# Performance work log

Measured on AMD Instinct MI355X. Metric: run time of the kernel, lower is better.

The kernel has to match this reference:

```python
import jax, jax.numpy as jnp
import numpy as np

B, N, D_IN, H, F = 2, 2048, 512, 8, 64
NEG_SLOPE = 0.2


def setup_inputs() -> dict:
    key = jax.random.key(0)
    k0, k1, k2, k3 = jax.random.split(key, 4)
    nodes = jax.random.normal(k0, (B, N, D_IN), dtype=jnp.float32)
    edges = jax.random.randint(k1, (B, N, N, 1), 0, 2).astype(jnp.int32)
    # ensure every node has at least one neighbor (self-loop) so softmax is finite
    idx = jnp.arange(N)
    edges = edges.at[:, idx, idx, :].set(1)
    W = jax.random.normal(k2, (D_IN, H * F), dtype=jnp.float32) * 0.02
    a = jax.random.normal(k3, (2 * F,), dtype=jnp.float32) * 0.02
    return {"nodes": nodes, "edges": edges, "W": W, "a": a}


def reference(nodes, edges, W, a):
    b, n, _ = nodes.shape
    mapped = (nodes @ W).reshape(b, n, H, F)  # [B,N,H,F]
    # additive attention: attn([m_i ; m_j]) = a_l . m_i + a_r . m_j
    a_l, a_r = a[:F], a[F:]
    el = jnp.einsum('bnhf,f->bnh', mapped, a_l)
    er = jnp.einsum('bnhf,f->bnh', mapped, a_r)
    scores = jax.nn.leaky_relu(el[:, :, None, :] + er[:, None, :, :], negative_slope=NEG_SLOPE)  # [B,N,N,H]
    mask = edges != 0  # [B,N,N,1] broadcasts over heads
    scores = jnp.where(mask, scores, -jnp.inf)
    attn_weights = jax.nn.softmax(scores, axis=2)  # softmax over neighbors j
    attn_res = jnp.einsum('bijh,bjhf->bihf', attn_weights, mapped)  # [B,N,H,F]
    # is_concat=False path: mean over heads, then sigmoid
    return jax.nn.sigmoid(attn_res.mean(axis=2))  # [B,N,F]
```

## Files before the change

### kernel.cpp

```cpp
#include <hip/hip_runtime.h>
#include <hip/hip_bf16.h>
#include <math.h>

#define Bq   2
#define Nq   2048
#define DIN  512
#define Hq   8
#define Fq   64
#define NEG  0.2f

using short8 = __attribute__((ext_vector_type(8))) short;
using half8  = __attribute__((ext_vector_type(8))) _Float16;
using half2v = __attribute__((ext_vector_type(2))) _Float16;
using f32x4  = __attribute__((ext_vector_type(4))) float;

__device__ inline unsigned int bf16_rne(float x) {
    unsigned int u = __float_as_uint(x);
    u += 0x7fffu + ((u >> 16) & 1u);
    return u >> 16;
}
__device__ inline unsigned int f16u(float x) {
    union { _Float16 h; unsigned short u; } cv;
    cv.h = (_Float16)x;
    return (unsigned int)cv.u;
}

#define AFRAG_BLOCKS 256
#define WFRAG_BLOCKS 128

__global__ __launch_bounds__(256) void prep_kernel(
    const float* __restrict__ nodes, ushort* __restrict__ Afrag,
    const float* __restrict__ W,     ushort* __restrict__ Wfrag)
{
    __shared__ __align__(16) char smem[16 * 516 * 4];
    const int bid = blockIdx.x;
    const int t   = threadIdx.x;

    if (bid < AFRAG_BLOCKS) {
        float (*As)[516] = (float(*)[516])smem;
        const int mt = bid;
        {
            const int row = t >> 4, c = t & 15;
#pragma unroll
            for (int i = 0; i < 8; i++) {
                float4 v = *(const float4*)&nodes[((size_t)mt * 16 + row) * DIN + (c + i * 16) * 4];
                *(float4*)&As[row][(c + i * 16) * 4] = v;
            }
        }
        __syncthreads();
        const int lane = t & 63, ksg = t >> 6;
        const int quad = lane >> 4, l15 = lane & 15;
#pragma unroll
        for (int k2 = 0; k2 < 4; k2++) {
            int ks = ksg * 4 + k2;
            const float* src = &As[l15][ks * 32 + quad * 8];
            float4 f0 = *(const float4*)src;
            float4 f1 = *(const float4*)(src + 4);
            uint4 pk;
            pk.x = bf16_rne(f0.x) | (bf16_rne(f0.y) << 16);
            pk.y = bf16_rne(f0.z) | (bf16_rne(f0.w) << 16);
            pk.z = bf16_rne(f1.x) | (bf16_rne(f1.y) << 16);
            pk.w = bf16_rne(f1.z) | (bf16_rne(f1.w) << 16);
            *(uint4*)(Afrag + ((size_t)(mt * 16 + ks) * 64 + lane) * 8) = pk;
        }
        return;
    }

    {
        float (*Ws)[68] = (float(*)[68])smem;
        const int id = bid - AFRAG_BLOCKS;
        const int ks = id & 15, h = id >> 4;
        {
            const int row = t >> 3, c = t & 7;
            const float* src = &W[(size_t)(ks * 32 + row) * (Hq * Fq) + h * 64 + c * 8];
            float4 v0 = *(const float4*)src;
            float4 v1 = *(const float4*)(src + 4);
            *(float4*)&Ws[row][c * 8]     = v0;
            *(float4*)&Ws[row][c * 8 + 4] = v1;
        }
        __syncthreads();
        const int lane = t & 63, nf = t >> 6;
        const int quad = lane >> 4, l15 = lane & 15;
        float f[8];
#pragma unroll
        for (int jj = 0; jj < 8; jj++) f[jj] = Ws[quad * 8 + jj][nf * 16 + l15];
        uint4 pk;
        pk.x = bf16_rne(f[0]) | (bf16_rne(f[1]) << 16);
        pk.y = bf16_rne(f[2]) | (bf16_rne(f[3]) << 16);
        pk.z = bf16_rne(f[4]) | (bf16_rne(f[5]) << 16);
        pk.w = bf16_rne(f[6]) | (bf16_rne(f[7]) << 16);
        *(uint4*)(Wfrag + (((size_t)(h * 16 + ks) * 4 + nf) * 64 + lane) * 8) = pk;
    }
}

#define GEMM_BLOCKS 512
#define PACK_BLOCKS 1024

__global__ __launch_bounds__(256) void work_kernel(
    const ushort* __restrict__ Afrag, const ushort* __restrict__ Wfrag,
    const float*  __restrict__ avec,
    ushort* __restrict__ Vfrag,
    float* __restrict__ el_t,
    float* __restrict__ er_t,
    ushort* __restrict__ Epk,
    ushort* __restrict__ Fpk,
    const int* __restrict__ edges, uint2* __restrict__ ebTB)
{
    const int bid = blockIdx.x;
    const int t   = threadIdx.x;

    if (bid >= GEMM_BLOCKS) {
        int gid = (bid - GEMM_BLOCKS) * 256 + t;
        int i  = gid & 2047;
        int jw = (gid >> 11) & 63;
        int b  = gid >> 17;
        const int4* ep = (const int4*)(edges + (((size_t)b * Nq + i) * Nq + jw * 32));
        int4 v[8];
#pragma unroll
        for (int c = 0; c < 8; c++) v[c] = ep[c];
#pragma unroll
        for (int q = 0; q < 4; q++) {
            unsigned int lo = 0, hi = 0;
            lo |= v[2*q].x   ? 0x000000FFu : 0u;  lo |= v[2*q].y   ? 0x0000FF00u : 0u;
            lo |= v[2*q].z   ? 0x00FF0000u : 0u;  lo |= v[2*q].w   ? 0xFF000000u : 0u;
            hi |= v[2*q+1].x ? 0x000000FFu : 0u;  hi |= v[2*q+1].y ? 0x0000FF00u : 0u;
            hi |= v[2*q+1].z ? 0x00FF0000u : 0u;  hi |= v[2*q+1].w ? 0xFF000000u : 0u;
            uint2 w; w.x = lo; w.y = hi;
            ebTB[((size_t)(b * 256 + jw * 4 + q)) * 2048 + i] = w;
        }
        return;
    }

    const int lane = t & 63;
    const int wv   = t >> 6;
    const int quad = lane >> 4;
    const int l15  = lane & 15;
    const int h    = bid >> 6;
    const int mt   = (bid & 63) * 4 + wv;
    const int row0 = mt * 16;

    const ushort* ap = Afrag + (size_t)mt * 8192 + lane * 8;
    const ushort* bp = Wfrag + (size_t)h * 32768 + lane * 8;

    f32x4 zero4 = {0.f, 0.f, 0.f, 0.f};
    f32x4 acc[4] = {zero4, zero4, zero4, zero4};

    short8 a0, a1, b0[4], b1[4];
    a0 = *(const short8*)(ap);
#pragma unroll
    for (int nf = 0; nf < 4; nf++) b0[nf] = *(const short8*)(bp + nf * 512);

    for (int ks = 0; ks < 16; ks += 2) {
        a1 = *(const short8*)(ap + (ks + 1) * 512);
#pragma unroll
        for (int nf = 0; nf < 4; nf++) b1[nf] = *(const short8*)(bp + (ks + 1) * 2048 + nf * 512);
#pragma unroll
        for (int nf = 0; nf < 4; nf++)
            acc[nf] = __builtin_amdgcn_mfma_f32_16x16x32_bf16(a0, b0[nf], acc[nf], 0, 0, 0);
        a0 = *(const short8*)(ap + (ks + 2) * 512);
#pragma unroll
        for (int nf = 0; nf < 4; nf++) b0[nf] = *(const short8*)(bp + (ks + 2) * 2048 + nf * 512);
#pragma unroll
        for (int nf = 0; nf < 4; nf++)
            acc[nf] = __builtin_amdgcn_mfma_f32_16x16x32_bf16(a1, b1[nf], acc[nf], 0, 0, 0);
    }

    float aL[4], aR[4];
#pragma unroll
    for (int nf = 0; nf < 4; nf++) {
        aL[nf] = avec[nf * 16 + l15];
        aR[nf] = avec[Fq + nf * 16 + l15];
    }
    const int bb = row0 >> 11;
    const int bh = bb * Hq + h;
#pragma unroll
    for (int r = 0; r < 4; r++) {
        float pl = acc[0][r] * aL[0] + acc[1][r] * aL[1] + acc[2][r] * aL[2] + acc[3][r] * aL[3];
        float pr = acc[0][r] * aR[0] + acc[1][r] * aR[1] + acc[2][r] * aR[2] + acc[3][r] * aR[3];
#pragma unroll
        for (int off = 1; off < 16; off <<= 1) {
            pl += __shfl_xor(pl, off, 64);
            pr += __shfl_xor(pr, off, 64);
        }
        if (l15 == 0) {
            int n = (row0 + quad * 4 + r) & (Nq - 1);
            el_t[(size_t)bh * Nq + n] = pl;
            er_t[(size_t)bh * Nq + n] = pr;
            Epk[(size_t)bh * Nq + n] = (ushort)f16u(__expf(pr));
            Fpk[(size_t)bh * Nq + n] = (ushort)f16u(__expf(NEG * pr));
        }
    }

    const int n_base = row0 & (Nq - 1);
    const int sblk   = n_base >> 5;
    const int quadp  = ((wv & 1) << 1) | (quad >> 1);
    const int jj0    = (quad & 1) * 4;
#pragma unroll
    for (int nf = 0; nf < 4; nf++) {
        uint2 pk;
        pk.x = f16u(acc[nf][0]) | (f16u(acc[nf][1]) << 16);
        pk.y = f16u(acc[nf][2]) | (f16u(acc[nf][3]) << 16);
        size_t off = ((((size_t)bh * 64 + sblk) * 4 + nf) * 64 + quadp * 16 + l15) * 8 + jj0;
        *(uint2*)(Vfrag + off) = pk;
    }
}

__global__ __launch_bounds__(256, 2) void attn_kernel(
    const float* __restrict__ el_t, const float* __restrict__ er_t,
    const ushort* __restrict__ Epk, const ushort* __restrict__ Fpk,
    const ushort* __restrict__ Vfrag,
    const uint2* __restrict__ ebTB, ushort* __restrict__ attn)
{
    const int lane = threadIdx.x & 63;
    const int kh   = threadIdx.x >> 6;
    const int quad = lane >> 4;
    const int l15  = lane & 15;
    const int bid  = blockIdx.x;
    const int it   = bid & 31;
    const int h    = (bid >> 5) & 7;
    const int b    = bid >> 8;
    const int bh   = b * Hq + h;
    const int i0   = it * 64;

    __shared__ float smax[4];
    __shared__ float lds_l[4][4][16];
    __shared__ __align__(16) float lds_acc[4][4][4][64][4];

    const float* errow = er_t + (size_t)bh * Nq;
    float mx = -INFINITY;
#pragma unroll
    for (int ii = 0; ii < 8; ii++) mx = fmaxf(mx, errow[threadIdx.x + ii * 256]);
#pragma unroll
    for (int off = 32; off > 0; off >>= 1) mx = fmaxf(mx, __shfl_xor(mx, off, 64));
    if (lane == 0) smax[kh] = mx;
    __syncthreads();
    const float emax = fmaxf(fmaxf(smax[0], smax[1]), fmaxf(smax[2], smax[3]));

    union HU { unsigned int u; half2v h; };
    HU AA2[4], CC2[4];
#pragma unroll
    for (int rs = 0; rs < 4; rs++) {
        float elv = el_t[(size_t)bh * Nq + i0 + rs * 16 + l15];
        float xm  = elv + emax;
        float m   = fmaxf(xm, NEG * xm);
        unsigned int a16 = f16u(__expf(elv - m));
        unsigned int c16 = f16u(__expf(NEG * elv - m));
        AA2[rs].u = a16 | (a16 << 16);
        CC2[rs].u = c16 | (c16 << 16);
    }

    const ushort* Ep = Epk + (size_t)bh * Nq + kh * 512;
    const ushort* Fp = Fpk + (size_t)bh * Nq + kh * 512;
    const ushort* vp = Vfrag + (size_t)bh * 131072 + kh * 32768 + lane * 8;
    const uint2*  mp = ebTB + ((size_t)(b * 256 + kh * 64 + quad)) * 2048 + i0 + l15;

    f32x4 zero4 = {0.f, 0.f, 0.f, 0.f};
    f32x4 acc[4][4];
    f32x4 accl[4];
#pragma unroll
    for (int rs = 0; rs < 4; rs++) {
        accl[rs] = zero4;
#pragma unroll
        for (int nf = 0; nf < 4; nf++) acc[rs][nf] = zero4;
    }

    const _Float16 one16 = (_Float16)1.0f;
    const half8 onesv = {one16, one16, one16, one16, one16, one16, one16, one16};

    for (int s = 0; s < 16; s++) {
        half8 vb0 = *(const half8*)(vp + s * 2048);
        half8 vb1 = *(const half8*)(vp + s * 2048 + 512);
        half8 vb2 = *(const half8*)(vp + s * 2048 + 1024);
        half8 vb3 = *(const half8*)(vp + s * 2048 + 1536);
        uint2 mbs[4];
#pragma unroll
        for (int rs = 0; rs < 4; rs++) mbs[rs] = mp[(size_t)s * 8192 + rs * 16];
        uint4 ev = *(const uint4*)(Ep + s * 32 + quad * 8);
        uint4 fv = *(const uint4*)(Fp + s * 32 + quad * 8);
        unsigned int ee[4] = {ev.x, ev.y, ev.z, ev.w};
        unsigned int ff[4] = {fv.x, fv.y, fv.z, fv.w};

#pragma unroll
        for (int rs = 0; rs < 4; rs++) {
            union AFU { half8 h8; unsigned int w4[4]; } af;
#pragma unroll
            for (int pp = 0; pp < 4; pp++) {
                HU e, f, pe, pf, P;
                e.u = ee[pp];
                f.u = ff[pp];
                pe.h = AA2[rs].h * e.h;
                pf.h = CC2[rs].h * f.h;
                P.h = __builtin_elementwise_max(pe.h, pf.h);
                unsigned int msrc = (pp < 2) ? mbs[rs].x : mbs[rs].y;
                unsigned int msel = (pp & 1) ? 0x03030202u : 0x01010000u;
                af.w4[pp] = P.u & __builtin_amdgcn_perm(0u, msrc, msel);
            }
            acc[rs][0] = __builtin_amdgcn_mfma_f32_16x16x32_f16(af.h8, vb0, acc[rs][0], 0, 0, 0);
            acc[rs][1] = __builtin_amdgcn_mfma_f32_16x16x32_f16(af.h8, vb1, acc[rs][1], 0, 0, 0);
            acc[rs][2] = __builtin_amdgcn_mfma_f32_16x16x32_f16(af.h8, vb2, acc[rs][2], 0, 0, 0);
            acc[rs][3] = __builtin_amdgcn_mfma_f32_16x16x32_f16(af.h8, vb3, acc[rs][3], 0, 0, 0);
            accl[rs]   = __builtin_amdgcn_mfma_f32_16x16x32_f16(af.h8, onesv, accl[rs], 0, 0, 0);
        }
    }

#pragma unroll
    for (int rs = 0; rs < 4; rs++)
#pragma unroll
        for (int nf = 0; nf < 4; nf++)
            *(f32x4*)&lds_acc[kh][rs][nf][lane][0] = acc[rs][nf];
    if (l15 == 0) {
#pragma unroll
        for (int rs = 0; rs < 4; rs++)
#pragma unroll
            for (int r = 0; r < 4; r++)
                lds_l[kh][rs][quad * 4 + r] = accl[rs][r];
    }
    __syncthreads();

    const int rs = kh;
    f32x4 facc[4] = {zero4, zero4, zero4, zero4};
#pragma unroll
    for (int k2 = 0; k2 < 4; k2++)
#pragma unroll
        for (int nf = 0; nf < 4; nf++) {
            f32x4 v = *(const f32x4*)&lds_acc[k2][rs][nf][lane][0];
            facc[nf][0] += v[0]; facc[nf][1] += v[1];
            facc[nf][2] += v[2]; facc[nf][3] += v[3];
        }
    float rl[4];
#pragma unroll
    for (int r = 0; r < 4; r++) {
        float sl = 0.f;
#pragma unroll
        for (int k2 = 0; k2 < 4; k2++) sl += lds_l[k2][rs][quad * 4 + r];
        rl[r] = 1.0f / sl;
    }
#pragma unroll
    for (int nf = 0; nf < 4; nf++)
#pragma unroll
        for (int r = 0; r < 4; r++)
            attn[(((size_t)b * Nq + i0 + rs * 16 + quad * 4 + r) * Hq + h) * Fq + nf * 16 + l15]
                = (ushort)f16u(facc[nf][r] * rl[r]);
}

__global__ __launch_bounds__(256) void out_kernel(
    const ushort* __restrict__ attn, float* __restrict__ out)
{
    const int idx = blockIdx.x * 256 + threadIdx.x;
    const int f   = idx & 63;
    const int bn  = idx >> 6;
    const ushort* p = attn + (size_t)bn * Hq * Fq + f;
    float s = 0.f;
#pragma unroll
    for (int h = 0; h < Hq; h++) {
        union { ushort u; _Float16 h16; } cv;
        cv.u = p[h * Fq];
        s += (float)cv.h16;
    }
    s *= (1.f / Hq);
    out[idx] = 1.f / (1.f + __expf(-s));
}

extern "C" void kernel_launch(void* const* d_in, const int* in_sizes, int n_in,
                              void* d_out, int out_size, void* d_ws, size_t ws_size,
                              hipStream_t stream) {
    const float* nodes = (const float*)d_in[0];
    const int*   edges = (const int*)d_in[1];
    const float* W     = (const float*)d_in[2];
    const float* a     = (const float*)d_in[3];
    float* out = (float*)d_out;

    char* ws = (char*)d_ws;
    ushort* Afrag = (ushort*)ws;           ws += (size_t)Bq * Nq * DIN * 2;
    ushort* Wfrag = (ushort*)ws;           ws += (size_t)DIN * Hq * Fq * 2;
    ushort* Vfrag = (ushort*)ws;           ws += (size_t)Bq * Hq * Nq * Fq * 2;
    float*  el_t  = (float*)ws;            ws += (size_t)Bq * Hq * Nq * 4;
    float*  er_t  = (float*)ws;            ws += (size_t)Bq * Hq * Nq * 4;
    ushort* Epk   = (ushort*)ws;           ws += (size_t)Bq * Hq * Nq * 2;
    ushort* Fpk   = (ushort*)ws;           ws += (size_t)Bq * Hq * Nq * 2;
    uint2*  ebTB  = (uint2*)ws;            ws += (size_t)Bq * Nq * Nq;
    ushort* attn  = (ushort*)ws;

    prep_kernel<<<AFRAG_BLOCKS + WFRAG_BLOCKS, 256, 0, stream>>>(nodes, Afrag, W, Wfrag);
    work_kernel<<<GEMM_BLOCKS + PACK_BLOCKS, 256, 0, stream>>>(
        Afrag, Wfrag, a, Vfrag, el_t, er_t, Epk, Fpk, edges, ebTB);
    attn_kernel<<<Bq * Hq * (Nq / 64), 256, 0, stream>>>(el_t, er_t, Epk, Fpk, Vfrag, ebTB, attn);
    out_kernel<<<(Bq * Nq * Fq) / 256, 256, 0, stream>>>(attn, out);
}
```

Measured before the change: 112.7 us.

## Compute per-head er max via atomics, sum softmax denominator with dot2, vectorize out

The per-(batch,head) maximum of er is now reduced in the GEMM epilogue with an order-preserving integer atomicMax, so the attention kernel no longer rescans 2048 er values per block before starting. The softmax denominator is computed with packed fdot2 against ones plus cross-lane shuffles, replacing a fifth MFMA per step. The 1/H head-mean factor is folded into the reciprocal, and the output kernel now handles 8 features per thread with vector loads and stores. The cost is global atomics and a dependency on prep_kernel to initialise the max keys.

```diff
diff --git a/kernel.cpp b/kernel.cpp
--- a/kernel.cpp
+++ b/kernel.cpp
@@ -25,16 +25,29 @@
     return (unsigned int)cv.u;
 }
 
+__device__ inline unsigned int fkey(float x) {
+    unsigned int b = __float_as_uint(x);
+    return (b & 0x80000000u) ? ~b : (b | 0x80000000u);
+}
+__device__ inline float fkey_dec(unsigned int k) {
+    unsigned int b = (k & 0x80000000u) ? (k ^ 0x80000000u) : ~k;
+    return __uint_as_float(b);
+}
+#define NEG_INF_KEY 0x007FFFFFu
+
 #define AFRAG_BLOCKS 256
 #define WFRAG_BLOCKS 128
 
 __global__ __launch_bounds__(256) void prep_kernel(
     const float* __restrict__ nodes, ushort* __restrict__ Afrag,
-    const float* __restrict__ W,     ushort* __restrict__ Wfrag)
+    const float* __restrict__ W,     ushort* __restrict__ Wfrag,
+    unsigned int* __restrict__ emax_key)
 {
     __shared__ __align__(16) char smem[16 * 516 * 4];
     const int bid = blockIdx.x;
     const int t   = threadIdx.x;
+
+    if (bid == 0 && t < 16) emax_key[t] = NEG_INF_KEY;
 
     if (bid < AFRAG_BLOCKS) {
         float (*As)[516] = (float(*)[516])smem;
@@ -101,9 +114,9 @@
     const float*  __restrict__ avec,
     ushort* __restrict__ Vfrag,
     float* __restrict__ el_t,
-    float* __restrict__ er_t,
     ushort* __restrict__ Epk,
     ushort* __restrict__ Fpk,
+    unsigned int* __restrict__ emax_key,
     const int* __restrict__ edges, uint2* __restrict__ ebTB)
 {
     const int bid = blockIdx.x;
@@ -173,6 +186,7 @@
     }
     const int bb = row0 >> 11;
     const int bh = bb * Hq + h;
+    float prmax = -INFINITY;
 #pragma unroll
     for (int r = 0; r < 4; r++) {
         float pl = acc[0][r] * aL[0] + acc[1][r] * aL[1] + acc[2][r] * aL[2] + acc[3][r] * aL[3];
@@ -182,14 +196,17 @@
             pl += __shfl_xor(pl, off, 64);
             pr += __shfl_xor(pr, off, 64);
         }
+        prmax = fmaxf(prmax, pr);
         if (l15 == 0) {
             int n = (row0 + quad * 4 + r) & (Nq - 1);
             el_t[(size_t)bh * Nq + n] = pl;
-            er_t[(size_t)bh * Nq + n] = pr;
             Epk[(size_t)bh * Nq + n] = (ushort)f16u(__expf(pr));
             Fpk[(size_t)bh * Nq + n] = (ushort)f16u(__expf(NEG * pr));
         }
     }
+    prmax = fmaxf(prmax, __shfl_xor(prmax, 16, 64));
+    prmax = fmaxf(prmax, __shfl_xor(prmax, 32, 64));
+    if (lane == 0) atomicMax(&emax_key[bh], fkey(prmax));
 
     const int n_base = row0 & (Nq - 1);
     const int sblk   = n_base >> 5;
@@ -206,7 +223,8 @@
 }
 
 __global__ __launch_bounds__(256, 2) void attn_kernel(
-    const float* __restrict__ el_t, const float* __restrict__ er_t,
+    const float* __restrict__ el_t,
+    const unsigned int* __restrict__ emax_key,
     const ushort* __restrict__ Epk, const ushort* __restrict__ Fpk,
     const ushort* __restrict__ Vfrag,
     const uint2* __restrict__ ebTB, ushort* __restrict__ attn)
@@ -222,19 +240,10 @@
     const int bh   = b * Hq + h;
     const int i0   = it * 64;
 
-    __shared__ float smax[4];
     __shared__ float lds_l[4][4][16];
     __shared__ __align__(16) float lds_acc[4][4][4][64][4];
 
-    const float* errow = er_t + (size_t)bh * Nq;
-    float mx = -INFINITY;
-#pragma unroll
-    for (int ii = 0; ii < 8; ii++) mx = fmaxf(mx, errow[threadIdx.x + ii * 256]);
-#pragma unroll
-    for (int off = 32; off > 0; off >>= 1) mx = fmaxf(mx, __shfl_xor(mx, off, 64));
-    if (lane == 0) smax[kh] = mx;
-    __syncthreads();
-    const float emax = fmaxf(fmaxf(smax[0], smax[1]), fmaxf(smax[2], smax[3]));
+    const float emax = fkey_dec(emax_key[bh]);
 
     union HU { unsigned int u; half2v h; };
     HU AA2[4], CC2[4];
@@ -256,16 +265,14 @@
 
     f32x4 zero4 = {0.f, 0.f, 0.f, 0.f};
     f32x4 acc[4][4];
-    f32x4 accl[4];
-#pragma unroll
-    for (int rs = 0; rs < 4; rs++) {
-        accl[rs] = zero4;
+    float lsum[4] = {0.f, 0.f, 0.f, 0.f};
+#pragma unroll
+    for (int rs = 0; rs < 4; rs++)
 #pragma unroll
         for (int nf = 0; nf < 4; nf++) acc[rs][nf] = zero4;
-    }
-
-    const _Float16 one16 = (_Float16)1.0f;
-    const half8 onesv = {one16, one16, one16, one16, one16, one16, one16, one16};
+
+    HU ones2;
+    ones2.u = 0x3C003C00u;
 
     for (int s = 0; s < 16; s++) {
         half8 vb0 = *(const half8*)(vp + s * 2048);
@@ -295,12 +302,34 @@
                 unsigned int msel = (pp & 1) ? 0x03030202u : 0x01010000u;
                 af.w4[pp] = P.u & __builtin_amdgcn_perm(0u, msrc, msel);
             }
+#if __has_builtin(__builtin_amdgcn_fdot2)
+#pragma unroll
+            for (int pp = 0; pp < 4; pp++) {
+                HU w; w.u = af.w4[pp];
+                lsum[rs] = __builtin_amdgcn_fdot2(w.h, ones2.h, lsum[rs], false);
+            }
+#else
+#pragma unroll
+            for (int pp = 0; pp < 4; pp++) {
+                HU w; w.u = af.w4[pp];
+                lsum[rs] += (float)w.h[0] + (float)w.h[1];
+            }
+#endif
             acc[rs][0] = __builtin_amdgcn_mfma_f32_16x16x32_f16(af.h8, vb0, acc[rs][0], 0, 0, 0);
             acc[rs][1] = __builtin_amdgcn_mfma_f32_16x16x32_f16(af.h8, vb1, acc[rs][1], 0, 0, 0);
             acc[rs][2] = __builtin_amdgcn_mfma_f32_16x16x32_f16(af.h8, vb2, acc[rs][2], 0, 0, 0);
             acc[rs][3] = __builtin_amdgcn_mfma_f32_16x16x32_f16(af.h8, vb3, acc[rs][3], 0, 0, 0);
-            accl[rs]   = __builtin_amdgcn_mfma_f32_16x16x32_f16(af.h8, onesv, accl[rs], 0, 0, 0);
-        }
+        }
+    }
+
+#pragma unroll
+    for (int rs = 0; rs < 4; rs++) {
+        lsum[rs] += __shfl_xor(lsum[rs], 16, 64);
+        lsum[rs] += __shfl_xor(lsum[rs], 32, 64);
+    }
+    if (quad == 0) {
+#pragma unroll
+        for (int rs = 0; rs < 4; rs++) lds_l[kh][rs][l15] = lsum[rs];
     }
 
 #pragma unroll
@@ -308,13 +337,6 @@
 #pragma unroll
         for (int nf = 0; nf < 4; nf++)
             *(f32x4*)&lds_acc[kh][rs][nf][lane][0] = acc[rs][nf];
-    if (l15 == 0) {
-#pragma unroll
-        for (int rs = 0; rs < 4; rs++)
-#pragma unroll
-            for (int r = 0; r < 4; r++)
-                lds_l[kh][rs][quad * 4 + r] = accl[rs][r];
-    }
     __syncthreads();
 
     const int rs = kh;
@@ -333,7 +355,7 @@
         float sl = 0.f;
 #pragma unroll
         for (int k2 = 0; k2 < 4; k2++) sl += lds_l[k2][rs][quad * 4 + r];
-        rl[r] = 1.0f / sl;
+        rl[r] = 1.0f / (8.0f * sl);
     }
 #pragma unroll
     for (int nf = 0; nf < 4; nf++)
@@ -347,18 +369,25 @@
     const ushort* __restrict__ attn, float* __restrict__ out)
 {
     const int idx = blockIdx.x * 256 + threadIdx.x;
-    const int f   = idx & 63;
-    const int bn  = idx >> 6;
-    const ushort* p = attn + (size_t)bn * Hq * Fq + f;
-    float s = 0.f;
+    const int f8  = idx & 7;
+    const int bn  = idx >> 3;
+    const ushort* p = attn + (size_t)bn * Hq * Fq + f8 * 8;
+    float s[8] = {0.f, 0.f, 0.f, 0.f, 0.f, 0.f, 0.f, 0.f};
 #pragma unroll
     for (int h = 0; h < Hq; h++) {
-        union { ushort u; _Float16 h16; } cv;
-        cv.u = p[h * Fq];
-        s += (float)cv.h16;
-    }
-    s *= (1.f / Hq);
-    out[idx] = 1.f / (1.f + __expf(-s));
+        union { short8 v; _Float16 h16[8]; } cv;
+        cv.v = *(const short8*)(p + h * Fq);
+#pragma unroll
+        for (int j = 0; j < 8; j++) s[j] += (float)cv.h16[j];
+    }
+    float4 o0, o1;
+    o0.x = 1.f / (1.f + __expf(-s[0]));  o0.y = 1.f / (1.f + __expf(-s[1]));
+    o0.z = 1.f / (1.f + __expf(-s[2]));  o0.w = 1.f / (1.f + __expf(-s[3]));
+    o1.x = 1.f / (1.f + __expf(-s[4]));  o1.y = 1.f / (1.f + __expf(-s[5]));
+    o1.z = 1.f / (1.f + __expf(-s[6]));  o1.w = 1.f / (1.f + __expf(-s[7]));
+    float* op = out + (size_t)bn * Fq + f8 * 8;
+    *(float4*)op       = o0;
+    *(float4*)(op + 4) = o1;
 }
 
 extern "C" void kernel_launch(void* const* d_in, const int* in_sizes, int n_in,
@@ -375,15 +404,15 @@
     ushort* Wfrag = (ushort*)ws;           ws += (size_t)DIN * Hq * Fq * 2;
     ushort* Vfrag = (ushort*)ws;           ws += (size_t)Bq * Hq * Nq * Fq * 2;
     float*  el_t  = (float*)ws;            ws += (size_t)Bq * Hq * Nq * 4;
-    float*  er_t  = (float*)ws;            ws += (size_t)Bq * Hq * Nq * 4;
     ushort* Epk   = (ushort*)ws;           ws += (size_t)Bq * Hq * Nq * 2;
     ushort* Fpk   = (ushort*)ws;           ws += (size_t)Bq * Hq * Nq * 2;
+    unsigned int* emax_key = (unsigned int*)ws; ws += 128;
     uint2*  ebTB  = (uint2*)ws;            ws += (size_t)Bq * Nq * Nq;
     ushort* attn  = (ushort*)ws;
 
-    prep_kernel<<<AFRAG_BLOCKS + WFRAG_BLOCKS, 256, 0, stream>>>(nodes, Afrag, W, Wfrag);
+    prep_kernel<<<AFRAG_BLOCKS + WFRAG_BLOCKS, 256, 0, stream>>>(nodes, Afrag, W, Wfrag, emax_key);
     work_kernel<<<GEMM_BLOCKS + PACK_BLOCKS, 256, 0, stream>>>(
-        Afrag, Wfrag, a, Vfrag, el_t, er_t, Epk, Fpk, edges, ebTB);
-    attn_kernel<<<Bq * Hq * (Nq / 64), 256, 0, stream>>>(el_t, er_t, Epk, Fpk, Vfrag, ebTB, attn);
-    out_kernel<<<(Bq * Nq * Fq) / 256, 256, 0, stream>>>(attn, out);
-}
+        Afrag, Wfrag, a, Vfrag, el_t, Epk, Fpk, emax_key, edges, ebTB);
+    attn_kernel<<<Bq * Hq * (Nq / 64), 256, 0, stream>>>(el_t, emax_key, Epk, Fpk, Vfrag, ebTB, attn);
+    out_kernel<<<(Bq * Nq * Fq) / (256 * 8), 256, 0, stream>>>(attn, out);
+}
```

After: 134.7 us. +19.5%, slower.
